# Optimization experiments

Hardware: AMD Instinct MI355X
Metric: run time of the kernel (lower is better)

The kernel has to match this reference:

```python
import jax, jax.numpy as jnp
import numpy as np

N, FIN, HID, HEADS, DHEAD = 4096, 512, 256, 4, 256
TOPK = 29  # hard-coded t=29 in HAN1.forward
FOUT = HEADS * DHEAD  # 1024


def setup_inputs() -> dict:
    key = jax.random.key(0)
    ks = jax.random.split(key, 12)
    h = jax.random.normal(ks[0], (N, FIN), dtype=jnp.float32)
    simlar = jax.random.normal(ks[1], (N, N), dtype=jnp.float32)
    # binary adjacency, avg degree ~41 so top-k (29) actually prunes
    adj = (jax.random.uniform(ks[2], (N, N)) < 0.01).astype(jnp.float32)
    s = 0.05
    W_trans = jax.random.normal(ks[3], (FIN, HID), dtype=jnp.float32) * s
    gat_W = jax.random.normal(ks[4], (HID, FOUT), dtype=jnp.float32) * s
    attn_l = jax.random.normal(ks[5], (HEADS, DHEAD), dtype=jnp.float32) * s
    attn_r = jax.random.normal(ks[6], (HEADS, DHEAD), dtype=jnp.float32) * s
    gat_bias = jnp.zeros((FOUT,), dtype=jnp.float32)
    sem_W1 = jax.random.normal(ks[7], (FOUT, 128), dtype=jnp.float32) * s
    sem_b1 = jnp.zeros((128,), dtype=jnp.float32)
    sem_W2 = jax.random.normal(ks[8], (128, 1), dtype=jnp.float32) * s
    return {"h": h, "simlar": simlar, "adj": adj, "W_trans": W_trans,
            "gat_W": gat_W, "attn_l": attn_l, "attn_r": attn_r,
            "gat_bias": gat_bias, "sem_W1": sem_W1, "sem_b1": sem_b1,
            "sem_W2": sem_W2}


def reference(h, simlar, adj, W_trans, gat_W, attn_l, attn_r, gat_bias,
              sem_W1, sem_b1, sem_W2):
    lrelu01 = lambda x: jax.nn.leaky_relu(x, 0.01)  # nn.LeakyReLU default
    # ---- adjacency sparsification: per-row top-k of filtered similarity ----
    filt = lrelu01(adj * simlar) * (adj > 0).astype(adj.dtype)  # [N,N]
    top_vals, top_idx = jax.lax.top_k(filt, TOPK)               # [N,TOPK]
    rows = jnp.arange(N)[:, None]
    newmat = jnp.zeros_like(filt).at[rows, top_idx].set(top_vals)
    mask = newmat != 0  # mask[src, dst]: edge src->dst (nonzero() semantics)
    # ---- feature transform (dropout p=0 -> identity) ----
    x = lrelu01(h @ W_trans)                                    # [N,HID]
    # ---- GATConv (DGL semantics, negative_slope=0.2, activation=elu) ----
    feat = (x @ gat_W).reshape(N, HEADS, DHEAD)                 # [N,H,D]
    el = jnp.einsum('nhd,hd->nh', feat, attn_l)                 # src scores
    er = jnp.einsum('nhd,hd->nh', feat, attn_r)                 # dst scores
    e = jax.nn.leaky_relu(el[:, None, :] + er[None, :, :], 0.2) # [src,dst,H]
    mask3 = mask[:, :, None]
    e = jnp.where(mask3, e, jnp.asarray(-1e30, e.dtype))
    emax = jnp.max(e, axis=0, keepdims=True)
    exp_e = jnp.where(mask3, jnp.exp(e - emax), 0.0)
    denom = jnp.sum(exp_e, axis=0, keepdims=True)
    alpha = exp_e / jnp.maximum(denom, 1e-20)  # zero-in-degree -> zero output
    rst = jnp.einsum('sdh,shf->dhf', alpha, feat)               # [N,H,D]
    rst = jax.nn.elu(rst + gat_bias.reshape(HEADS, DHEAD))
    sem = rst.reshape(N, FOUT)                                  # flatten(1)
    # ---- semantic attention over meta-paths (here: 1 meta-path) ----
    z = sem[:, None, :]                                         # [N,1,F]
    w = (jnp.tanh(z @ sem_W1 + sem_b1) @ sem_W2).mean(0)        # [1,1]
    beta = jax.nn.softmax(w, axis=0)                            # [1,1]
    out = (beta[None, :, :] * z).sum(1)                         # [N,F]
    return out
```

## Files before the change

### kernel.cpp

```cpp
#include <hip/hip_runtime.h>
#include <hip/hip_bf16.h>
#include <math.h>

#define N 4096
#define FIN 512
#define HID 256
#define HEADS 4
#define DHEAD 256
#define FOUT 1024
#define TOPK 29
#define CAP 64
#define CAPC 96

typedef __attribute__((ext_vector_type(8))) short short8;
typedef __attribute__((ext_vector_type(4))) float f32x4;
typedef __hip_bfloat16 bf16;

__device__ __forceinline__ float bflo(unsigned int u) {
  return __uint_as_float(u << 16);
}
__device__ __forceinline__ float bfhi(unsigned int u) {
  return __uint_as_float(u & 0xffff0000u);
}

__global__ __launch_bounds__(256) void scan_kernel(
    const float* __restrict__ W_trans, const float* __restrict__ gat_W,
    const float* __restrict__ attn_l, const float* __restrict__ attn_r,
    const float* __restrict__ adj, const float* __restrict__ simlar,
    bf16* __restrict__ Wtb, bf16* __restrict__ gWtb,
    float* __restrict__ alr2, int* __restrict__ colcnt,
    int* __restrict__ colsrc) {
  const int t = threadIdx.x, s = blockIdx.x;
  {
    const int S1 = 4096;
    const int S2 = S1 + HID * FIN / 4;
    const int S3 = S2 + FOUT * HID / 4;
    const int TOT = S3 + 2 * HEADS * HID * 16;
    const int i = s * 256 + t;
    if (i < TOT) {
      if (i < S1) {
        colcnt[i] = 0;
      } else if (i < S2) {
        const int j4 = i - S1;
        const float4 v = reinterpret_cast<const float4*>(W_trans)[j4];
        const int k = j4 >> 6;
        const int c0 = (j4 & 63) * 4;
        Wtb[(size_t)(c0 + 0) * FIN + k] = __float2bfloat16(v.x);
        Wtb[(size_t)(c0 + 1) * FIN + k] = __float2bfloat16(v.y);
        Wtb[(size_t)(c0 + 2) * FIN + k] = __float2bfloat16(v.z);
        Wtb[(size_t)(c0 + 3) * FIN + k] = __float2bfloat16(v.w);
      } else if (i < S3) {
        const int j4 = i - S2;
        const float4 v = reinterpret_cast<const float4*>(gat_W)[j4];
        const int k = j4 >> 8;
        const int c0 = (j4 & 255) * 4;
        gWtb[(size_t)(c0 + 0) * HID + k] = __float2bfloat16(v.x);
        gWtb[(size_t)(c0 + 1) * HID + k] = __float2bfloat16(v.y);
        gWtb[(size_t)(c0 + 2) * HID + k] = __float2bfloat16(v.z);
        gWtb[(size_t)(c0 + 3) * HID + k] = __float2bfloat16(v.w);
      } else {
        const int u = i - S3;
        const int j = u >> 4, l16 = u & 15;
        const float* vec = (j < 1024) ? attn_l : attn_r;
        const int jj = j & 1023;
        const int hh = jj >> 8, k = jj & 255;
        const float4* wp = reinterpret_cast<const float4*>(
            &gat_W[(size_t)k * FOUT + hh * DHEAD + l16 * 16]);
        const float4* vp = reinterpret_cast<const float4*>(&vec[hh * DHEAD + l16 * 16]);
        float acc = 0.f;
#pragma unroll
        for (int q = 0; q < 4; ++q) {
          const float4 w4 = wp[q], v4 = vp[q];
          acc += w4.x * v4.x + w4.y * v4.y + w4.z * v4.z + w4.w * v4.w;
        }
#pragma unroll
        for (int off = 1; off < 16; off <<= 1) acc += __shfl_xor(acc, off);
        if (l16 == 0) alr2[j] = acc;
      }
    }
  }
  __shared__ float swv[CAP];
  __shared__ int swi[CAP];
  __shared__ int cnt;
  if (t == 0) cnt = 0;
  __syncthreads();
  const uint4* rowadj = reinterpret_cast<const uint4*>(adj + (size_t)s * N);
  const float4* rowsim = reinterpret_cast<const float4*>(simlar + (size_t)s * N);
  uint4 a[4];
#pragma unroll
  for (int q = 0; q < 4; ++q) a[q] = rowadj[q * 256 + t];
  bool ghit[4];
#pragma unroll
  for (int q = 0; q < 4; ++q) ghit[q] = (a[q].x | a[q].y | a[q].z | a[q].w) != 0;
  float4 sv[4];
#pragma unroll
  for (int q = 0; q < 4; ++q) {
    if (ghit[q]) sv[q] = rowsim[q * 256 + t];
  }
#pragma unroll
  for (int q = 0; q < 4; ++q) {
    if (ghit[q]) {
      const int j = q * 256 + t;
      const unsigned aw[4] = {a[q].x, a[q].y, a[q].z, a[q].w};
      const float ss[4] = {sv[q].x, sv[q].y, sv[q].z, sv[q].w};
#pragma unroll
      for (int c = 0; c < 4; ++c) {
        if (aw[c] && ss[c] > 0.f) {
          const int p = atomicAdd(&cnt, 1);
          if (p < CAP) {
            swv[p] = ss[c];
            swi[p] = j * 4 + c;
          }
        }
      }
    }
  }
  __syncthreads();
  const int C = min(cnt, CAP);
  if (t < C) {
    const float x = swv[t];
    int rk = 0;
    for (int jj = 0; jj < C; ++jj) rk += (swv[jj] > x);
    if (rk < TOPK) {
      const int d = swi[t];
      const int p = atomicAdd(&colcnt[d], 1);
      if (p < CAPC) colsrc[(size_t)d * CAPC + p] = s;
    }
  }
}

__global__ __launch_bounds__(256) void gemm_h(const float* __restrict__ A,
                                              const bf16* __restrict__ Bt,
                                              bf16* __restrict__ Cb) {
  __shared__ bf16 As[64][72];
  __shared__ bf16 Bs[64][72];
  const int t = threadIdx.x;
  const int bm = blockIdx.x * 64, bn = blockIdx.y * 64;
  const int w = t >> 6, lane = t & 63, r = lane & 15, g = lane >> 4;
  const int m = t >> 2;
  const int fb = (t & 3) * 16;
  const int c0 = (t & 3) * 8;
  f32x4 acc[4] = {};
  for (int k0 = 0; k0 < FIN; k0 += 64) {
    {
      const float4* hp = reinterpret_cast<const float4*>(&A[(size_t)(bm + m) * FIN + k0 + fb]);
      const float4 f0 = hp[0], f1 = hp[1], f2 = hp[2], f3 = hp[3];
      bf16 ta[16];
      ta[0] = __float2bfloat16(f0.x); ta[1] = __float2bfloat16(f0.y);
      ta[2] = __float2bfloat16(f0.z); ta[3] = __float2bfloat16(f0.w);
      ta[4] = __float2bfloat16(f1.x); ta[5] = __float2bfloat16(f1.y);
      ta[6] = __float2bfloat16(f1.z); ta[7] = __float2bfloat16(f1.w);
      ta[8] = __float2bfloat16(f2.x); ta[9] = __float2bfloat16(f2.y);
      ta[10] = __float2bfloat16(f2.z); ta[11] = __float2bfloat16(f2.w);
      ta[12] = __float2bfloat16(f3.x); ta[13] = __float2bfloat16(f3.y);
      ta[14] = __float2bfloat16(f3.z); ta[15] = __float2bfloat16(f3.w);
      *reinterpret_cast<int4*>(&As[m][fb]) = *reinterpret_cast<int4*>(&ta[0]);
      *reinterpret_cast<int4*>(&As[m][fb + 8]) = *reinterpret_cast<int4*>(&ta[8]);
    }
    {
      const bf16* brow = &Bt[(size_t)(bn + m) * FIN + k0];
      *reinterpret_cast<int4*>(&Bs[m][c0]) = *reinterpret_cast<const int4*>(&brow[c0]);
      *reinterpret_cast<int4*>(&Bs[m][c0 + 32]) = *reinterpret_cast<const int4*>(&brow[c0 + 32]);
    }
    __syncthreads();
    const short8 a0 = *reinterpret_cast<short8*>(&As[w * 16 + r][g * 8]);
    const short8 a1 = *reinterpret_cast<short8*>(&As[w * 16 + r][32 + g * 8]);
#pragma unroll
    for (int j = 0; j < 4; ++j) {
      const short8 b0 = *reinterpret_cast<short8*>(&Bs[j * 16 + r][g * 8]);
      const short8 b1 = *reinterpret_cast<short8*>(&Bs[j * 16 + r][32 + g * 8]);
      acc[j] = __builtin_amdgcn_mfma_f32_16x16x32_bf16(a0, b0, acc[j], 0, 0, 0);
      acc[j] = __builtin_amdgcn_mfma_f32_16x16x32_bf16(a1, b1, acc[j], 0, 0, 0);
    }
    __syncthreads();
  }
#pragma unroll
  for (int j = 0; j < 4; ++j)
#pragma unroll
    for (int q = 0; q < 4; ++q) {
      const int row = bm + w * 16 + g * 4 + q;
      const int col = bn + j * 16 + r;
      float v = acc[j][q];
      v = v >= 0.f ? v : 0.01f * v;
      Cb[(size_t)row * HID + col] = __float2bfloat16(v);
    }
}

__global__ __launch_bounds__(256) void gemm128(const bf16* __restrict__ A,
                                               const bf16* __restrict__ Bt,
                                               bf16* __restrict__ Cb) {
  __shared__ bf16 As[128][72];
  __shared__ bf16 Bs[128][72];
  const int t = threadIdx.x;
  const int bm = blockIdx.x * 128, bn = blockIdx.y * 128;
  const int w = t >> 6, lane = t & 63, r = lane & 15, g = lane >> 4;
  const int m = t >> 1, cb = (t & 1) * 32;
  f32x4 acc[2][8] = {};
  for (int k0 = 0; k0 < HID; k0 += 64) {
    const bf16* arow = &A[(size_t)(bm + m) * HID + k0 + cb];
    const bf16* brow = &Bt[(size_t)(bn + m) * HID + k0 + cb];
#pragma unroll
    for (int q = 0; q < 4; ++q) {
      *reinterpret_cast<int4*>(&As[m][cb + q * 8]) =
          *reinterpret_cast<const int4*>(&arow[q * 8]);
      *reinterpret_cast<int4*>(&Bs[m][cb + q * 8]) =
          *reinterpret_cast<const int4*>(&brow[q * 8]);
    }
    __syncthreads();
    const short8 a00 = *reinterpret_cast<short8*>(&As[w * 32 + r][g * 8]);
    const short8 a01 = *reinterpret_cast<short8*>(&As[w * 32 + r][32 + g * 8]);
    const short8 a10 = *reinterpret_cast<short8*>(&As[w * 32 + 16 + r][g * 8]);
    const short8 a11 = *reinterpret_cast<short8*>(&As[w * 32 + 16 + r][32 + g * 8]);
#pragma unroll
    for (int j = 0; j < 8; ++j) {
      const short8 b0 = *reinterpret_cast<short8*>(&Bs[j * 16 + r][g * 8]);
      const short8 b1 = *reinterpret_cast<short8*>(&Bs[j * 16 + r][32 + g * 8]);
      acc[0][j] = __builtin_amdgcn_mfma_f32_16x16x32_bf16(a00, b0, acc[0][j], 0, 0, 0);
      acc[0][j] = __builtin_amdgcn_mfma_f32_16x16x32_bf16(a01, b1, acc[0][j], 0, 0, 0);
      acc[1][j] = __builtin_amdgcn_mfma_f32_16x16x32_bf16(a10, b0, acc[1][j], 0, 0, 0);
      acc[1][j] = __builtin_amdgcn_mfma_f32_16x16x32_bf16(a11, b1, acc[1][j], 0, 0, 0);
    }
    __syncthreads();
  }
  const int hh = bn >> 8;
  const int dbase = bn & 255;
#pragma unroll
  for (int i = 0; i < 2; ++i)
#pragma unroll
    for (int j = 0; j < 8; ++j)
#pragma unroll
      for (int q = 0; q < 4; ++q) {
        const int row = bm + w * 32 + i * 16 + g * 4 + q;
        const int dd = dbase + j * 16 + r;
        Cb[((size_t)hh * N + row) * DHEAD + dd] = __float2bfloat16(acc[i][j][q]);
      }
}

__global__ __launch_bounds__(256) void elr2_kernel(const bf16* __restrict__ xb,
                                                   const float* __restrict__ alr2,
                                                   float* __restrict__ el,
                                                   float* __restrict__ er) {
  __shared__ float alrs[2048];
  const int t = threadIdx.x;
  for (int i = t; i < 2048; i += 256) alrs[i] = alr2[i];
  __syncthreads();
  const int wv = t >> 6, lane = t & 63;
  const int n = blockIdx.x * 4 + wv;
  const uint2 v2 = *reinterpret_cast<const uint2*>(&xb[(size_t)n * HID + lane * 4]);
  const float xf[4] = {bflo(v2.x), bfhi(v2.x), bflo(v2.y), bfhi(v2.y)};
  float pl[4], pr[4];
#pragma unroll
  for (int hh = 0; hh < 4; ++hh) {
    const int base = hh * 256 + lane * 4;
    pl[hh] = xf[0] * alrs[base] + xf[1] * alrs[base + 1] +
             xf[2] * alrs[base + 2] + xf[3] * alrs[base + 3];
    pr[hh] = xf[0] * alrs[1024 + base] + xf[1] * alrs[1024 + base + 1] +
             xf[2] * alrs[1024 + base + 2] + xf[3] * alrs[1024 + base + 3];
  }
  for (int off = 32; off; off >>= 1) {
#pragma unroll
    for (int hh = 0; hh < 4; ++hh) {
      pl[hh] += __shfl_xor(pl[hh], off);
      pr[hh] += __shfl_xor(pr[hh], off);
    }
  }
  if (lane == 0) {
#pragma unroll
    for (int hh = 0; hh < 4; ++hh) {
      el[n * HEADS + hh] = pl[hh];
      er[n * HEADS + hh] = pr[hh];
    }
  }
}

__global__ __launch_bounds__(256) void agg_kernel(const int* __restrict__ colcnt,
                                                  const int* __restrict__ colsrc,
                                                  const float* __restrict__ el,
                                                  const float* __restrict__ er,
                                                  const bf16* __restrict__ featb,
                                                  const float* __restrict__ bias,
                                                  float* __restrict__ out) {
  __shared__ int tmp[4][CAPC];
  __shared__ int slist[4][CAPC];
  __shared__ float pbuf[4][CAPC];
  const int t = threadIdx.x;
  const int grp = t >> 6;
  const int lane = t & 63;
  const int h = blockIdx.x & 3;
  const int d = (blockIdx.x >> 2) * 4 + grp;
  const int C = min(colcnt[d], CAPC);
  for (int i = lane; i < C; i += 64) tmp[grp][i] = colsrc[(size_t)d * CAPC + i];
  for (int i = lane; i < C; i += 64) {
    const int v = tmp[grp][i];
    int rk = 0;
    for (int j = 0; j < C; ++j) rk += (tmp[grp][j] < v);
    slist[grp][rk] = v;
  }
  const float er_dh = er[d * HEADS + h];
  float m = -INFINITY;
  for (int i = lane; i < C; i += 64) {
    float e = el[slist[grp][i] * HEADS + h] + er_dh;
    e = e >= 0.f ? e : 0.2f * e;
    pbuf[grp][i] = e;
    m = fmaxf(m, e);
  }
#pragma unroll
  for (int off = 32; off; off >>= 1) m = fmaxf(m, __shfl_xor(m, off));
  float dsum = 0.f;
  for (int i = lane; i < C; i += 64) {
    const float p = __expf(pbuf[grp][i] - m);
    pbuf[grp][i] = p;
    dsum += p;
  }
#pragma unroll
  for (int off = 32; off; off >>= 1) dsum += __shfl_xor(dsum, off);
  const bf16* fh = featb + (size_t)h * N * DHEAD;
  float a0 = 0.f, a1 = 0.f, a2 = 0.f, a3 = 0.f;
  int i = 0;
  for (; i + 4 <= C; i += 4) {
    const float p0 = pbuf[grp][i];
    const float p1 = pbuf[grp][i + 1];
    const float p2 = pbuf[grp][i + 2];
    const float p3 = pbuf[grp][i + 3];
    const uint2 v0 = *reinterpret_cast<const uint2*>(
        &fh[(size_t)slist[grp][i] * DHEAD + lane * 4]);
    const uint2 v1 = *reinterpret_cast<const uint2*>(
        &fh[(size_t)slist[grp][i + 1] * DHEAD + lane * 4]);
    const uint2 v2 = *reinterpret_cast<const uint2*>(
        &fh[(size_t)slist[grp][i + 2] * DHEAD + lane * 4]);
    const uint2 v3 = *reinterpret_cast<const uint2*>(
        &fh[(size_t)slist[grp][i + 3] * DHEAD + lane * 4]);
    a0 = fmaf(p0, bflo(v0.x), a0);
    a1 = fmaf(p0, bfhi(v0.x), a1);
    a2 = fmaf(p0, bflo(v0.y), a2);
    a3 = fmaf(p0, bfhi(v0.y), a3);
    a0 = fmaf(p1, bflo(v1.x), a0);
    a1 = fmaf(p1, bfhi(v1.x), a1);
    a2 = fmaf(p1, bflo(v1.y), a2);
    a3 = fmaf(p1, bfhi(v1.y), a3);
    a0 = fmaf(p2, bflo(v2.x), a0);
    a1 = fmaf(p2, bfhi(v2.x), a1);
    a2 = fmaf(p2, bflo(v2.y), a2);
    a3 = fmaf(p2, bfhi(v2.y), a3);
    a0 = fmaf(p3, bflo(v3.x), a0);
    a1 = fmaf(p3, bfhi(v3.x), a1);
    a2 = fmaf(p3, bflo(v3.y), a2);
    a3 = fmaf(p3, bfhi(v3.y), a3);
  }
  for (; i < C; ++i) {
    const float p0 = pbuf[grp][i];
    const uint2 v0 = *reinterpret_cast<const uint2*>(
        &fh[(size_t)slist[grp][i] * DHEAD + lane * 4]);
    a0 = fmaf(p0, bflo(v0.x), a0);
    a1 = fmaf(p0, bfhi(v0.x), a1);
    a2 = fmaf(p0, bflo(v0.y), a2);
    a3 = fmaf(p0, bfhi(v0.y), a3);
  }
  const float inv = C > 0 ? 1.f / dsum : 0.f;
  const int dbase = h * DHEAD + lane * 4;
  float o[4];
  o[0] = a0 * inv + bias[dbase + 0];
  o[1] = a1 * inv + bias[dbase + 1];
  o[2] = a2 * inv + bias[dbase + 2];
  o[3] = a3 * inv + bias[dbase + 3];
#pragma unroll
  for (int k = 0; k < 4; ++k) o[k] = o[k] > 0.f ? o[k] : expm1f(o[k]);
  *reinterpret_cast<float4*>(&out[(size_t)d * FOUT + dbase]) =
      make_float4(o[0], o[1], o[2], o[3]);
}

extern "C" void kernel_launch(void* const* d_in, const int* in_sizes, int n_in,
                              void* d_out, int out_size, void* d_ws, size_t ws_size,
                              hipStream_t stream) {
  const float* h        = (const float*)d_in[0];
  const float* simlar   = (const float*)d_in[1];
  const float* adj      = (const float*)d_in[2];
  const float* W_trans  = (const float*)d_in[3];
  const float* gat_W    = (const float*)d_in[4];
  const float* attn_l   = (const float*)d_in[5];
  const float* attn_r   = (const float*)d_in[6];
  const float* gat_bias = (const float*)d_in[7];
  float* out = (float*)d_out;

  char* ws = (char*)d_ws;
  const size_t MB = 1 << 20;
  bf16* Wtb   = (bf16*)(ws);
  bf16* gWtb  = (bf16*)(ws + 512 * 1024);
  bf16* xb    = (bf16*)(ws + 1 * MB);
  float* el   = (float*)(ws + 3 * MB);
  float* er   = (float*)(ws + 3 * MB + 65536);
  float* alr2 = (float*)(ws + 3 * MB + 131072);
  bf16* featb = (bf16*)(ws + 4 * MB);
  int* colcnt = (int*)(ws + 12 * MB);
  int* colsrc = (int*)(ws + 13 * MB);

  scan_kernel<<<N, 256, 0, stream>>>(W_trans, gat_W, attn_l, attn_r, adj, simlar,
                                     Wtb, gWtb, alr2, colcnt, colsrc);
  gemm_h<<<dim3(N / 64, HID / 64), 256, 0, stream>>>(h, Wtb, xb);
  gemm128<<<dim3(N / 128, FOUT / 128), 256, 0, stream>>>(xb, gWtb, featb);
  elr2_kernel<<<N / 4, 256, 0, stream>>>(xb, alr2, el, er);
  agg_kernel<<<N, 256, 0, stream>>>(colcnt, colsrc, el, er, featb, gat_bias, out);
}
```

Before: 64.88 us.

## Fuse both GEMMs and attention-score projection into one row-block kernel

Replaces the three kernels gemm_h, gemm128 and elr2 with a single kernel. Each 512-thread block handles 16 rows: it computes x = lrelu(h@W_trans) into LDS, derives el/er from x, then computes feat = x@gat_W directly from LDS. This removes the xb round trip through global memory and two launches. In exchange, B operands are read straight from global/L2 without LDS staging, only 256 blocks of small 16-row tiles are launched, and the weight matrices get re-read by every block.

New measurement: 76.25 us. 17.5% more time.

```diff
diff --git a/kernel.cpp b/kernel.cpp
--- a/kernel.cpp
+++ b/kernel.cpp
@@ -129,146 +129,99 @@
   }
 }
 
-__global__ __launch_bounds__(256) void gemm_h(const float* __restrict__ A,
-                                              const bf16* __restrict__ Bt,
-                                              bf16* __restrict__ Cb) {
-  __shared__ bf16 As[64][72];
-  __shared__ bf16 Bs[64][72];
+__global__ __launch_bounds__(512) void xfeat_kernel(
+    const float* __restrict__ h, const bf16* __restrict__ Wtb,
+    const bf16* __restrict__ gWtb, const float* __restrict__ alr2,
+    float* __restrict__ el, float* __restrict__ er,
+    bf16* __restrict__ featb) {
+  __shared__ __align__(16) bf16 xs[16][264];
+  __shared__ float alrs[2048];
   const int t = threadIdx.x;
-  const int bm = blockIdx.x * 64, bn = blockIdx.y * 64;
+  const int bm = blockIdx.x * 16;
   const int w = t >> 6, lane = t & 63, r = lane & 15, g = lane >> 4;
-  const int m = t >> 2;
-  const int fb = (t & 3) * 16;
-  const int c0 = (t & 3) * 8;
-  f32x4 acc[4] = {};
-  for (int k0 = 0; k0 < FIN; k0 += 64) {
-    {
-      const float4* hp = reinterpret_cast<const float4*>(&A[(size_t)(bm + m) * FIN + k0 + fb]);
-      const float4 f0 = hp[0], f1 = hp[1], f2 = hp[2], f3 = hp[3];
-      bf16 ta[16];
+  for (int i = t; i < 2048; i += 512) alrs[i] = alr2[i];
+  {
+    f32x4 acc[2] = {};
+    const float* hrow = &h[(size_t)(bm + r) * FIN];
+#pragma unroll 4
+    for (int k0 = 0; k0 < FIN; k0 += 32) {
+      const float4 f0 = *reinterpret_cast<const float4*>(&hrow[k0 + g * 8]);
+      const float4 f1 = *reinterpret_cast<const float4*>(&hrow[k0 + g * 8 + 4]);
+      bf16 ta[8];
       ta[0] = __float2bfloat16(f0.x); ta[1] = __float2bfloat16(f0.y);
       ta[2] = __float2bfloat16(f0.z); ta[3] = __float2bfloat16(f0.w);
       ta[4] = __float2bfloat16(f1.x); ta[5] = __float2bfloat16(f1.y);
       ta[6] = __float2bfloat16(f1.z); ta[7] = __float2bfloat16(f1.w);
-      ta[8] = __float2bfloat16(f2.x); ta[9] = __float2bfloat16(f2.y);
-      ta[10] = __float2bfloat16(f2.z); ta[11] = __float2bfloat16(f2.w);
-      ta[12] = __float2bfloat16(f3.x); ta[13] = __float2bfloat16(f3.y);
-      ta[14] = __float2bfloat16(f3.z); ta[15] = __float2bfloat16(f3.w);
-      *reinterpret_cast<int4*>(&As[m][fb]) = *reinterpret_cast<int4*>(&ta[0]);
-      *reinterpret_cast<int4*>(&As[m][fb + 8]) = *reinterpret_cast<int4*>(&ta[8]);
-    }
-    {
-      const bf16* brow = &Bt[(size_t)(bn + m) * FIN + k0];
-      *reinterpret_cast<int4*>(&Bs[m][c0]) = *reinterpret_cast<const int4*>(&brow[c0]);
-      *reinterpret_cast<int4*>(&Bs[m][c0 + 32]) = *reinterpret_cast<const int4*>(&brow[c0 + 32]);
-    }
-    __syncthreads();
-    const short8 a0 = *reinterpret_cast<short8*>(&As[w * 16 + r][g * 8]);
-    const short8 a1 = *reinterpret_cast<short8*>(&As[w * 16 + r][32 + g * 8]);
-#pragma unroll
-    for (int j = 0; j < 4; ++j) {
-      const short8 b0 = *reinterpret_cast<short8*>(&Bs[j * 16 + r][g * 8]);
-      const short8 b1 = *reinterpret_cast<short8*>(&Bs[j * 16 + r][32 + g * 8]);
-      acc[j] = __builtin_amdgcn_mfma_f32_16x16x32_bf16(a0, b0, acc[j], 0, 0, 0);
-      acc[j] = __builtin_amdgcn_mfma_f32_16x16x32_bf16(a1, b1, acc[j], 0, 0, 0);
-    }
-    __syncthreads();
-  }
-#pragma unroll
-  for (int j = 0; j < 4; ++j)
-#pragma unroll
-    for (int q = 0; q < 4; ++q) {
-      const int row = bm + w * 16 + g * 4 + q;
-      const int col = bn + j * 16 + r;
-      float v = acc[j][q];
-      v = v >= 0.f ? v : 0.01f * v;
-      Cb[(size_t)row * HID + col] = __float2bfloat16(v);
-    }
-}
-
-__global__ __launch_bounds__(256) void gemm128(const bf16* __restrict__ A,
-                                               const bf16* __restrict__ Bt,
-                                               bf16* __restrict__ Cb) {
-  __shared__ bf16 As[128][72];
-  __shared__ bf16 Bs[128][72];
-  const int t = threadIdx.x;
-  const int bm = blockIdx.x * 128, bn = blockIdx.y * 128;
-  const int w = t >> 6, lane = t & 63, r = lane & 15, g = lane >> 4;
-  const int m = t >> 1, cb = (t & 1) * 32;
-  f32x4 acc[2][8] = {};
-  for (int k0 = 0; k0 < HID; k0 += 64) {
-    const bf16* arow = &A[(size_t)(bm + m) * HID + k0 + cb];
-    const bf16* brow = &Bt[(size_t)(bn + m) * HID + k0 + cb];
-#pragma unroll
-    for (int q = 0; q < 4; ++q) {
-      *reinterpret_cast<int4*>(&As[m][cb + q * 8]) =
-          *reinterpret_cast<const int4*>(&arow[q * 8]);
-      *reinterpret_cast<int4*>(&Bs[m][cb + q * 8]) =
-          *reinterpret_cast<const int4*>(&brow[q * 8]);
-    }
-    __syncthreads();
-    const short8 a00 = *reinterpret_cast<short8*>(&As[w * 32 + r][g * 8]);
-    const short8 a01 = *reinterpret_cast<short8*>(&As[w * 32 + r][32 + g * 8]);
-    const short8 a10 = *reinterpret_cast<short8*>(&As[w * 32 + 16 + r][g * 8]);
-    const short8 a11 = *reinterpret_cast<short8*>(&As[w * 32 + 16 + r][32 + g * 8]);
+      const short8 av = *reinterpret_cast<short8*>(ta);
+#pragma unroll
+      for (int j = 0; j < 2; ++j) {
+        const int row = w * 32 + j * 16 + r;
+        const short8 bv = *reinterpret_cast<const short8*>(
+            &Wtb[(size_t)row * FIN + k0 + g * 8]);
+        acc[j] = __builtin_amdgcn_mfma_f32_16x16x32_bf16(av, bv, acc[j], 0, 0, 0);
+      }
+    }
+#pragma unroll
+    for (int j = 0; j < 2; ++j)
+#pragma unroll
+      for (int q = 0; q < 4; ++q) {
+        float v = acc[j][q];
+        v = v >= 0.f ? v : 0.01f * v;
+        xs[g * 4 + q][w * 32 + j * 16 + r] = __float2bfloat16(v);
+      }
+  }
+  __syncthreads();
+  {
+    const int row = w * 2 + (lane >> 5);
+    const int kl = (lane & 31) * 8;
+    float pl[4] = {}, pr[4] = {};
+#pragma unroll
+    for (int e = 0; e < 8; ++e) {
+      const float xv = __bfloat162float(xs[row][kl + e]);
+#pragma unroll
+      for (int hh = 0; hh < 4; ++hh) {
+        pl[hh] = fmaf(xv, alrs[hh * 256 + kl + e], pl[hh]);
+        pr[hh] = fmaf(xv, alrs[1024 + hh * 256 + kl + e], pr[hh]);
+      }
+    }
+#pragma unroll
+    for (int off = 1; off < 32; off <<= 1) {
+#pragma unroll
+      for (int hh = 0; hh < 4; ++hh) {
+        pl[hh] += __shfl_xor(pl[hh], off);
+        pr[hh] += __shfl_xor(pr[hh], off);
+      }
+    }
+    if ((lane & 31) == 0) {
+#pragma unroll
+      for (int hh = 0; hh < 4; ++hh) {
+        el[(bm + row) * HEADS + hh] = pl[hh];
+        er[(bm + row) * HEADS + hh] = pr[hh];
+      }
+    }
+  }
+  {
+    f32x4 acc[8] = {};
+#pragma unroll 2
+    for (int k0 = 0; k0 < HID; k0 += 32) {
+      const short8 av = *reinterpret_cast<short8*>(&xs[r][k0 + g * 8]);
+#pragma unroll
+      for (int j = 0; j < 8; ++j) {
+        const int grow = w * 128 + j * 16 + r;
+        const short8 bv = *reinterpret_cast<const short8*>(
+            &gWtb[(size_t)grow * HID + k0 + g * 8]);
+        acc[j] = __builtin_amdgcn_mfma_f32_16x16x32_bf16(av, bv, acc[j], 0, 0, 0);
+      }
+    }
 #pragma unroll
     for (int j = 0; j < 8; ++j) {
-      const short8 b0 = *reinterpret_cast<short8*>(&Bs[j * 16 + r][g * 8]);
-      const short8 b1 = *reinterpret_cast<short8*>(&Bs[j * 16 + r][32 + g * 8]);
-      acc[0][j] = __builtin_amdgcn_mfma_f32_16x16x32_bf16(a00, b0, acc[0][j], 0, 0, 0);
-      acc[0][j] = __builtin_amdgcn_mfma_f32_16x16x32_bf16(a01, b1, acc[0][j], 0, 0, 0);
-      acc[1][j] = __builtin_amdgcn_mfma_f32_16x16x32_bf16(a10, b0, acc[1][j], 0, 0, 0);
-      acc[1][j] = __builtin_amdgcn_mfma_f32_16x16x32_bf16(a11, b1, acc[1][j], 0, 0, 0);
-    }
-    __syncthreads();
-  }
-  const int hh = bn >> 8;
-  const int dbase = bn & 255;
-#pragma unroll
-  for (int i = 0; i < 2; ++i)
-#pragma unroll
-    for (int j = 0; j < 8; ++j)
+      const int col = w * 128 + j * 16 + r;
+      const int hh = col >> 8, dd = col & 255;
 #pragma unroll
       for (int q = 0; q < 4; ++q) {
-        const int row = bm + w * 32 + i * 16 + g * 4 + q;
-        const int dd = dbase + j * 16 + r;
-        Cb[((size_t)hh * N + row) * DHEAD + dd] = __float2bfloat16(acc[i][j][q]);
-      }
-}
-
-__global__ __launch_bounds__(256) void elr2_kernel(const bf16* __restrict__ xb,
-                                                   const float* __restrict__ alr2,
-                                                   float* __restrict__ el,
-                                                   float* __restrict__ er) {
-  __shared__ float alrs[2048];
-  const int t = threadIdx.x;
-  for (int i = t; i < 2048; i += 256) alrs[i] = alr2[i];
-  __syncthreads();
-  const int wv = t >> 6, lane = t & 63;
-  const int n = blockIdx.x * 4 + wv;
-  const uint2 v2 = *reinterpret_cast<const uint2*>(&xb[(size_t)n * HID + lane * 4]);
-  const float xf[4] = {bflo(v2.x), bfhi(v2.x), bflo(v2.y), bfhi(v2.y)};
-  float pl[4], pr[4];
-#pragma unroll
-  for (int hh = 0; hh < 4; ++hh) {
-    const int base = hh * 256 + lane * 4;
-    pl[hh] = xf[0] * alrs[base] + xf[1] * alrs[base + 1] +
-             xf[2] * alrs[base + 2] + xf[3] * alrs[base + 3];
-    pr[hh] = xf[0] * alrs[1024 + base] + xf[1] * alrs[1024 + base + 1] +
-             xf[2] * alrs[1024 + base + 2] + xf[3] * alrs[1024 + base + 3];
-  }
-  for (int off = 32; off; off >>= 1) {
-#pragma unroll
-    for (int hh = 0; hh < 4; ++hh) {
-      pl[hh] += __shfl_xor(pl[hh], off);
-      pr[hh] += __shfl_xor(pr[hh], off);
-    }
-  }
-  if (lane == 0) {
-#pragma unroll
-    for (int hh = 0; hh < 4; ++hh) {
-      el[n * HEADS + hh] = pl[hh];
-      er[n * HEADS + hh] = pr[hh];
+        featb[((size_t)hh * N + bm + g * 4 + q) * DHEAD + dd] =
+            __float2bfloat16(acc[j][q]);
+      }
     }
   }
 }
@@ -386,7 +339,6 @@
   const size_t MB = 1 << 20;
   bf16* Wtb   = (bf16*)(ws);
   bf16* gWtb  = (bf16*)(ws + 512 * 1024);
-  bf16* xb    = (bf16*)(ws + 1 * MB);
   float* el   = (float*)(ws + 3 * MB);
   float* er   = (float*)(ws + 3 * MB + 65536);
   float* alr2 = (float*)(ws + 3 * MB + 131072);
@@ -396,8 +348,6 @@
 
   scan_kernel<<<N, 256, 0, stream>>>(W_trans, gat_W, attn_l, attn_r, adj, simlar,
                                      Wtb, gWtb, alr2, colcnt, colsrc);
-  gemm_h<<<dim3(N / 64, HID / 64), 256, 0, stream>>>(h, Wtb, xb);
-  gemm128<<<dim3(N / 128, FOUT / 128), 256, 0, stream>>>(xb, gWtb, featb);
-  elr2_kernel<<<N / 4, 256, 0, stream>>>(xb, alr2, el, er);
+  xfeat_kernel<<<N / 16, 512, 0, stream>>>(h, Wtb, gWtb, alr2, el, er, featb);
   agg_kernel<<<N, 256, 0, stream>>>(colcnt, colsrc, el, er, featb, gat_bias, out);
 }
```
